# Kernel tuning notes

Hardware: AMD Instinct MI355X
Metric: run time of the kernel (lower is better)

The kernel has to match this reference:

```python
import jax, jax.numpy as jnp
import numpy as np

S = 64.0   # arcface scale
M = 0.5    # arcface additive angular margin
EPS = 1e-07
B, D, C = 1024, 512, 100000


def setup_inputs() -> dict:
    key = jax.random.key(0)
    k1, k2, k3 = jax.random.split(key, 3)
    features = jax.random.normal(k1, (B, D), dtype=jnp.float32)
    # Linear(512, 100000, bias=False) weight, ~1/sqrt(512) init scale.
    W = jax.random.normal(k2, (C, D), dtype=jnp.float32) * 0.04
    y_true = jax.random.randint(k3, (B,), 0, C, dtype=jnp.int64)
    return {"features": features, "W": W, "y_true": y_true}


def reference(features, W, y_true):
    # L2-normalize features along dim=1 (torch F.normalize, eps=1e-12).
    norm = jnp.maximum(jnp.linalg.norm(features, axis=1, keepdims=True), 1e-12)
    xn = features / norm
    # NOTE: the original module's weight-normalization loop is a no-op
    # (rebinds a local), so W is used unnormalized — faithful to the source.
    wf = xn @ W.T                                   # [B, C] cosine-like logits
    tgt = wf[jnp.arange(B), y_true]                  # true-class logit per row
    # arcface: s * cos(acos(clamp(t)) + m)
    numerator = S * jnp.cos(jnp.arccos(jnp.clip(tgt, -1.0 + EPS, 1.0 - EPS)) + M)
    # exp-sum over all classes except the true one (mask instead of python-loop concat)
    not_true = jnp.arange(C)[None, :] != y_true[:, None]   # [B, C]
    excl_sum = jnp.sum(jnp.where(not_true, jnp.exp(S * wf), 0.0), axis=1)
    denominator = jnp.exp(numerator) + excl_sum
    L = numerator - jnp.log(denominator)
    return -jnp.mean(L)
```

## Files before the change

kernel.cpp:

```cpp
#include <hip/hip_runtime.h>
#include <math.h>

#define BATCH 1024
#define DIM   512
#define NCLS  100000
#define SCALE_S 64.0f
#define MARGIN  0.5f
#define EPS_REF 1e-7f
#define NBLK 782
#define MBLK 8
#define BKF8 128
#define WCVT_BLKS 25000
#define SEXP 92.332482616893656878f

typedef __attribute__((ext_vector_type(4))) float floatx4;

#if __has_builtin(__builtin_amdgcn_exp2f)
#define EXP2(x) __builtin_amdgcn_exp2f(x)
#else
#define EXP2(x) exp2f(x)
#endif

__device__ __forceinline__ void gload_lds16(const void* g, void* l) {
    __builtin_amdgcn_global_load_lds(
        (const __attribute__((address_space(1))) void*)g,
        (__attribute__((address_space(3))) void*)l, 16, 0, 0);
}

__global__ __launch_bounds__(256)
void k_cvtprep(const float* __restrict__ W,
               const float* __restrict__ features,
               const int* __restrict__ y,
               unsigned char* __restrict__ wf8,
               unsigned char* __restrict__ xf8,
               float* __restrict__ rowsum,
               float* __restrict__ tgt) {
    const int b = blockIdx.x;
    if (b < WCVT_BLKS) {
        const size_t i = ((size_t)b * 256 + threadIdx.x) * 8;
        const float4 lo = *(const float4*)(W + i);
        const float4 hi = *(const float4*)(W + i + 4);
        int p0 = __builtin_amdgcn_cvt_pk_fp8_f32(lo.x, lo.y, 0, false);
        p0     = __builtin_amdgcn_cvt_pk_fp8_f32(lo.z, lo.w, p0, true);
        int p1 = __builtin_amdgcn_cvt_pk_fp8_f32(hi.x, hi.y, 0, false);
        p1     = __builtin_amdgcn_cvt_pk_fp8_f32(hi.z, hi.w, p1, true);
        *(int2*)(wf8 + i) = make_int2(p0, p1);
    } else {
        const int row = b - WCVT_BLKS;
        const int t = threadIdx.x;
        const int lane = t & 63;
        const int wave = t >> 6;
        __shared__ float redS[4], redD[4];

        const float2 v  = *(const float2*)(features + (size_t)row * DIM + t * 2);
        const float2 wv = *(const float2*)(W + (size_t)y[row] * DIM + t * 2);
        float ss = v.x * v.x + v.y * v.y;
        float dd = v.x * wv.x + v.y * wv.y;
        #pragma unroll
        for (int m = 32; m >= 1; m >>= 1) { ss += __shfl_xor(ss, m); dd += __shfl_xor(dd, m); }
        if (lane == 0) { redS[wave] = ss; redD[wave] = dd; }
        __syncthreads();
        const float tot  = redS[0] + redS[1] + redS[2] + redS[3];
        const float dtot = redD[0] + redD[1] + redD[2] + redD[3];
        const float nrm = fmaxf(sqrtf(tot), 1e-12f);
        const float sc = SEXP / nrm;

        int pk = __builtin_amdgcn_cvt_pk_fp8_f32(v.x * sc, v.y * sc, 0, false);
        *(unsigned short*)(xf8 + (size_t)row * DIM + t * 2) = (unsigned short)(pk & 0xFFFF);

        if (t == 0) { rowsum[row] = 0.0f; tgt[row] = dtot / nrm; }
    }
}

__global__ __launch_bounds__(256)
void k_gemm_f8(const unsigned char* __restrict__ wf8,
               const unsigned char* __restrict__ xf8,
               float* __restrict__ rowsum) {
    __shared__ __align__(16) unsigned char As[128 * BKF8];
    __shared__ __align__(16) unsigned char Bs[128 * BKF8];

    const int tid  = threadIdx.x;
    const int wave = tid >> 6;
    const int lane = tid & 63;
    const int quad = lane >> 4;
    const int l15  = lane & 15;
    const int wm   = wave >> 1;
    const int wn   = wave & 1;

    const int bid = blockIdx.x;
    const int xcd = bid & 7;
    const int j   = bid >> 3;
    const int w   = xcd * NBLK + j;
    const int n_blk = w >> 3;
    const int m_blk = w & 7;
    const int n0 = n_blk * 128;
    const int m0 = m_blk * 128;

    const int rl = lane >> 3;
    const int cs = lane & 7;
    const unsigned char* a_src[4];
    const unsigned char* b_src[4];
    unsigned char* a_dst[4];
    unsigned char* b_dst[4];
    #pragma unroll
    for (int i = 0; i < 4; ++i) {
        const int r = wave * 32 + i * 8 + rl;
        a_src[i] = xf8 + (size_t)(m0 + r) * DIM + (cs ^ rl) * 16;
        int n = n0 + r;
        if (n > NCLS - 1) n = NCLS - 1;
        b_src[i] = wf8 + (size_t)n * DIM + (cs ^ rl) * 16;
        a_dst[i] = &As[(wave * 32 + i * 8) * BKF8];
        b_dst[i] = &Bs[(wave * 32 + i * 8) * BKF8];
    }

    int aoff[4], boff[4];
    #pragma unroll
    for (int mi = 0; mi < 4; ++mi) {
        const int r = wm * 64 + mi * 16 + l15;
        aoff[mi] = r * BKF8 + (((quad >> 1) ^ (r & 7)) * 16) + (quad & 1) * 8;
    }
    #pragma unroll
    for (int ni = 0; ni < 4; ++ni) {
        const int r = wn * 64 + ni * 16 + l15;
        boff[ni] = r * BKF8 + (((quad >> 1) ^ (r & 7)) * 16) + (quad & 1) * 8;
    }

    floatx4 acc[4][4];
    #pragma unroll
    for (int i = 0; i < 4; ++i)
        #pragma unroll
        for (int jj = 0; jj < 4; ++jj)
            acc[i][jj] = (floatx4){0.f, 0.f, 0.f, 0.f};

    for (int kt = 0; kt < DIM / BKF8; ++kt) {
        __syncthreads();
        #pragma unroll
        for (int i = 0; i < 4; ++i) {
            gload_lds16(a_src[i] + kt * BKF8, a_dst[i]);
            gload_lds16(b_src[i] + kt * BKF8, b_dst[i]);
        }
        __syncthreads();

        #pragma unroll
        for (int kc = 0; kc < 4; ++kc) {
            long a[4], b[4];
            #pragma unroll
            for (int mi = 0; mi < 4; ++mi)
                a[mi] = *(const long*)(&As[aoff[mi] ^ (kc << 5)]);
            #pragma unroll
            for (int ni = 0; ni < 4; ++ni)
                b[ni] = *(const long*)(&Bs[boff[ni] ^ (kc << 5)]);
            #pragma unroll
            for (int mi = 0; mi < 4; ++mi)
                #pragma unroll
                for (int ni = 0; ni < 4; ++ni)
                    acc[mi][ni] = __builtin_amdgcn_mfma_f32_16x16x32_fp8_fp8(
                        a[mi], b[ni], acc[mi][ni], 0, 0, 0);
        }
    }

    const bool full = (n0 + 128 <= NCLS);
    #pragma unroll
    for (int mi = 0; mi < 4; ++mi) {
        #pragma unroll
        for (int reg = 0; reg < 4; ++reg) {
            float p = 0.f;
            if (full) {
                #pragma unroll
                for (int ni = 0; ni < 4; ++ni)
                    p += EXP2(acc[mi][ni][reg]);
            } else {
                #pragma unroll
                for (int ni = 0; ni < 4; ++ni) {
                    const int n = n0 + wn * 64 + ni * 16 + l15;
                    if (n < NCLS) p += EXP2(acc[mi][ni][reg]);
                }
            }
            p += __shfl_xor(p, 1);
            p += __shfl_xor(p, 2);
            p += __shfl_xor(p, 4);
            p += __shfl_xor(p, 8);
            if (l15 == 0) {
                const int m = m0 + wm * 64 + mi * 16 + quad * 4 + reg;
                atomicAdd(&rowsum[m], p);
            }
        }
    }
}

__global__ void k_finalize(const float* __restrict__ rowsum,
                           const float* __restrict__ tgt,
                           float* __restrict__ out) {
    const int tid = threadIdx.x;
    const int lane = tid & 63;
    const int wave = tid >> 6;
    __shared__ float red[4];

    float s = 0.f;
    #pragma unroll
    for (int i = 0; i < 4; ++i) {
        const int b = tid + i * 256;
        const float traw = tgt[b];
        const float tc = fminf(fmaxf(traw, -1.0f + EPS_REF), 1.0f - EPS_REF);
        const float num = SCALE_S * cosf(acosf(tc) + MARGIN);
        const float excl = rowsum[b] - expf(SCALE_S * traw);
        const float denom = expf(num) + excl;
        s += num - logf(denom);
    }
    #pragma unroll
    for (int m = 32; m >= 1; m >>= 1) s += __shfl_xor(s, m);
    if (lane == 0) red[wave] = s;
    __syncthreads();
    if (tid == 0)
        out[0] = -(red[0] + red[1] + red[2] + red[3]) / (float)BATCH;
}

extern "C" void kernel_launch(void* const* d_in, const int* in_sizes, int n_in,
                              void* d_out, int out_size, void* d_ws, size_t ws_size,
                              hipStream_t stream) {
    const float* features = (const float*)d_in[0];
    const float* W        = (const float*)d_in[1];
    const int*   y        = (const int*)d_in[2];
    float* out = (float*)d_out;

    const size_t WF8_BYTES = (size_t)NCLS * DIM;
    const size_t XF8_BYTES = (size_t)BATCH * DIM;
    char* ws = (char*)d_ws;
    unsigned char* wf8 = (unsigned char*)ws;
    unsigned char* xf8 = (unsigned char*)(ws + WF8_BYTES);
    float* rowsum = (float*)(ws + WF8_BYTES + XF8_BYTES);
    float* tgt    = (float*)(ws + WF8_BYTES + XF8_BYTES + 4096);

    k_cvtprep<<<WCVT_BLKS + BATCH, 256, 0, stream>>>(W, features, y,
                                                     wf8, xf8, rowsum, tgt);
    k_gemm_f8<<<NBLK * MBLK, 256, 0, stream>>>(wf8, xf8, rowsum);
    k_finalize<<<1, 256, 0, stream>>>(rowsum, tgt, out);
}
```

Measured before the change: 453.3 us.

## Fuse W fp8 conversion into GEMM with LDS-resident weight slabs

Removes the separate pass that converts W to fp8 and writes it back to a workspace. Each GEMM block now loads a 64-row slab of fp32 W, converts it to fp8 in LDS once, and keeps it resident while it streams all 1024 feature rows through a double-buffered LDS tile. This avoids writing and re-reading the 51 MB fp8 copy of W, so W's fp32 bytes are read only once. In exchange, every block re-reads the whole fp8 feature matrix, the tiles are smaller (64 columns, 2x4 MFMAs per wave), and each block issues more atomics.

```diff
diff --git a/kernel.cpp b/kernel.cpp
--- a/kernel.cpp
+++ b/kernel.cpp
@@ -7,11 +7,14 @@
 #define SCALE_S 64.0f
 #define MARGIN  0.5f
 #define EPS_REF 1e-7f
-#define NBLK 782
-#define MBLK 8
-#define BKF8 128
-#define WCVT_BLKS 25000
 #define SEXP 92.332482616893656878f
+
+#define NSLAB 64
+#define NBLK  1563
+#define BK    64
+#define NKT   8
+#define MROWS 128
+#define NMT   8
 
 typedef __attribute__((ext_vector_type(4))) float floatx4;
 
@@ -28,161 +31,158 @@
 }
 
 __global__ __launch_bounds__(256)
-void k_cvtprep(const float* __restrict__ W,
-               const float* __restrict__ features,
-               const int* __restrict__ y,
-               unsigned char* __restrict__ wf8,
-               unsigned char* __restrict__ xf8,
-               float* __restrict__ rowsum,
-               float* __restrict__ tgt) {
-    const int b = blockIdx.x;
-    if (b < WCVT_BLKS) {
-        const size_t i = ((size_t)b * 256 + threadIdx.x) * 8;
-        const float4 lo = *(const float4*)(W + i);
-        const float4 hi = *(const float4*)(W + i + 4);
-        int p0 = __builtin_amdgcn_cvt_pk_fp8_f32(lo.x, lo.y, 0, false);
-        p0     = __builtin_amdgcn_cvt_pk_fp8_f32(lo.z, lo.w, p0, true);
-        int p1 = __builtin_amdgcn_cvt_pk_fp8_f32(hi.x, hi.y, 0, false);
-        p1     = __builtin_amdgcn_cvt_pk_fp8_f32(hi.z, hi.w, p1, true);
-        *(int2*)(wf8 + i) = make_int2(p0, p1);
-    } else {
-        const int row = b - WCVT_BLKS;
-        const int t = threadIdx.x;
-        const int lane = t & 63;
-        const int wave = t >> 6;
-        __shared__ float redS[4], redD[4];
-
-        const float2 v  = *(const float2*)(features + (size_t)row * DIM + t * 2);
-        const float2 wv = *(const float2*)(W + (size_t)y[row] * DIM + t * 2);
-        float ss = v.x * v.x + v.y * v.y;
-        float dd = v.x * wv.x + v.y * wv.y;
-        #pragma unroll
-        for (int m = 32; m >= 1; m >>= 1) { ss += __shfl_xor(ss, m); dd += __shfl_xor(dd, m); }
-        if (lane == 0) { redS[wave] = ss; redD[wave] = dd; }
-        __syncthreads();
-        const float tot  = redS[0] + redS[1] + redS[2] + redS[3];
-        const float dtot = redD[0] + redD[1] + redD[2] + redD[3];
-        const float nrm = fmaxf(sqrtf(tot), 1e-12f);
-        const float sc = SEXP / nrm;
-
-        int pk = __builtin_amdgcn_cvt_pk_fp8_f32(v.x * sc, v.y * sc, 0, false);
-        *(unsigned short*)(xf8 + (size_t)row * DIM + t * 2) = (unsigned short)(pk & 0xFFFF);
-
-        if (t == 0) { rowsum[row] = 0.0f; tgt[row] = dtot / nrm; }
-    }
-}
-
-__global__ __launch_bounds__(256)
-void k_gemm_f8(const unsigned char* __restrict__ wf8,
-               const unsigned char* __restrict__ xf8,
-               float* __restrict__ rowsum) {
-    __shared__ __align__(16) unsigned char As[128 * BKF8];
-    __shared__ __align__(16) unsigned char Bs[128 * BKF8];
+void k_prep(const float* __restrict__ features,
+            const float* __restrict__ W,
+            const int* __restrict__ y,
+            unsigned char* __restrict__ xf8,
+            float* __restrict__ rowsum,
+            float* __restrict__ tgt) {
+    const int row = blockIdx.x;
+    const int t = threadIdx.x;
+    const int lane = t & 63;
+    const int wave = t >> 6;
+    __shared__ float redS[4], redD[4];
+
+    const float2 v  = *(const float2*)(features + (size_t)row * DIM + t * 2);
+    const float2 wv = *(const float2*)(W + (size_t)y[row] * DIM + t * 2);
+    float ss = v.x * v.x + v.y * v.y;
+    float dd = v.x * wv.x + v.y * wv.y;
+    #pragma unroll
+    for (int m = 32; m >= 1; m >>= 1) { ss += __shfl_xor(ss, m); dd += __shfl_xor(dd, m); }
+    if (lane == 0) { redS[wave] = ss; redD[wave] = dd; }
+    __syncthreads();
+    const float tot  = redS[0] + redS[1] + redS[2] + redS[3];
+    const float dtot = redD[0] + redD[1] + redD[2] + redD[3];
+    const float nrm = fmaxf(sqrtf(tot), 1e-12f);
+    const float sc = SEXP / nrm;
+
+    int pk = __builtin_amdgcn_cvt_pk_fp8_f32(v.x * sc, v.y * sc, 0, false);
+    *(unsigned short*)(xf8 + (size_t)row * DIM + t * 2) = (unsigned short)(pk & 0xFFFF);
+
+    if (t == 0) { rowsum[row] = 0.0f; tgt[row] = dtot / nrm; }
+}
+
+__global__ __launch_bounds__(256, 3)
+void k_gemm_fused(const float* __restrict__ W,
+                  const unsigned char* __restrict__ xf8,
+                  float* __restrict__ rowsum) {
+    __shared__ __align__(16) unsigned char Ws[NSLAB * DIM];
+    __shared__ __align__(16) unsigned char As[2][MROWS * BK];
 
     const int tid  = threadIdx.x;
     const int wave = tid >> 6;
     const int lane = tid & 63;
     const int quad = lane >> 4;
     const int l15  = lane & 15;
-    const int wm   = wave >> 1;
-    const int wn   = wave & 1;
-
-    const int bid = blockIdx.x;
-    const int xcd = bid & 7;
-    const int j   = bid >> 3;
-    const int w   = xcd * NBLK + j;
-    const int n_blk = w >> 3;
-    const int m_blk = w & 7;
-    const int n0 = n_blk * 128;
-    const int m0 = m_blk * 128;
-
-    const int rl = lane >> 3;
-    const int cs = lane & 7;
-    const unsigned char* a_src[4];
-    const unsigned char* b_src[4];
-    unsigned char* a_dst[4];
-    unsigned char* b_dst[4];
-    #pragma unroll
-    for (int i = 0; i < 4; ++i) {
-        const int r = wave * 32 + i * 8 + rl;
-        a_src[i] = xf8 + (size_t)(m0 + r) * DIM + (cs ^ rl) * 16;
-        int n = n0 + r;
-        if (n > NCLS - 1) n = NCLS - 1;
-        b_src[i] = wf8 + (size_t)n * DIM + (cs ^ rl) * 16;
-        a_dst[i] = &As[(wave * 32 + i * 8) * BKF8];
-        b_dst[i] = &Bs[(wave * 32 + i * 8) * BKF8];
-    }
-
-    int aoff[4], boff[4];
-    #pragma unroll
-    for (int mi = 0; mi < 4; ++mi) {
-        const int r = wm * 64 + mi * 16 + l15;
-        aoff[mi] = r * BKF8 + (((quad >> 1) ^ (r & 7)) * 16) + (quad & 1) * 8;
+    const int n0   = blockIdx.x * NSLAB;
+
+    const int arl = lane >> 2;
+    const int acs = lane & 3;
+    const unsigned char* a_src_base =
+        xf8 + (size_t)arl * DIM + ((acs ^ (arl & 3)) << 4);
+
+    #pragma unroll
+    for (int q = 0; q < 2; ++q)
+        gload_lds16(a_src_base + (size_t)((q * 4 + wave) * 16) * DIM,
+                    &As[0][(q * 4 + wave) * 16 * BK]);
+
+    #pragma unroll
+    for (int j = 0; j < 8; ++j) {
+        const int c  = j * 256 + tid;
+        const int r  = c >> 5;
+        const int cs = c & 31;
+        int rg = n0 + r; if (rg > NCLS - 1) rg = NCLS - 1;
+        const float4* s4 = (const float4*)(W + (size_t)rg * DIM + cs * 16);
+        const float4 f0 = s4[0], f1 = s4[1], f2 = s4[2], f3 = s4[3];
+        int w0 = __builtin_amdgcn_cvt_pk_fp8_f32(f0.x, f0.y, 0, false);
+        w0     = __builtin_amdgcn_cvt_pk_fp8_f32(f0.z, f0.w, w0, true);
+        int w1 = __builtin_amdgcn_cvt_pk_fp8_f32(f1.x, f1.y, 0, false);
+        w1     = __builtin_amdgcn_cvt_pk_fp8_f32(f1.z, f1.w, w1, true);
+        int w2 = __builtin_amdgcn_cvt_pk_fp8_f32(f2.x, f2.y, 0, false);
+        w2     = __builtin_amdgcn_cvt_pk_fp8_f32(f2.z, f2.w, w2, true);
+        int w3 = __builtin_amdgcn_cvt_pk_fp8_f32(f3.x, f3.y, 0, false);
+        w3     = __builtin_amdgcn_cvt_pk_fp8_f32(f3.z, f3.w, w3, true);
+        *(int4*)(&Ws[r * DIM + ((cs ^ (r & 7)) << 4)]) = make_int4(w0, w1, w2, w3);
+    }
+
+    int aoff[2], boff[4];
+    #pragma unroll
+    for (int mi = 0; mi < 2; ++mi) {
+        const int r = wave * 32 + mi * 16 + l15;
+        aoff[mi] = r * BK + (((quad >> 1) ^ (r & 3)) << 4) + ((quad & 1) << 3);
     }
     #pragma unroll
     for (int ni = 0; ni < 4; ++ni) {
-        const int r = wn * 64 + ni * 16 + l15;
-        boff[ni] = r * BKF8 + (((quad >> 1) ^ (r & 7)) * 16) + (quad & 1) * 8;
-    }
-
-    floatx4 acc[4][4];
-    #pragma unroll
-    for (int i = 0; i < 4; ++i)
+        const int r = ni * 16 + l15;
+        boff[ni] = r * DIM + (((quad >> 1) ^ (r & 7)) << 4) + ((quad & 1) << 3);
+    }
+
+    floatx4 acc[2][4];
+    int buf = 0;
+    const bool full = (n0 + NSLAB <= NCLS);
+
+    for (int mt = 0; mt < NMT; ++mt) {
         #pragma unroll
-        for (int jj = 0; jj < 4; ++jj)
-            acc[i][jj] = (floatx4){0.f, 0.f, 0.f, 0.f};
-
-    for (int kt = 0; kt < DIM / BKF8; ++kt) {
-        __syncthreads();
-        #pragma unroll
-        for (int i = 0; i < 4; ++i) {
-            gload_lds16(a_src[i] + kt * BKF8, a_dst[i]);
-            gload_lds16(b_src[i] + kt * BKF8, b_dst[i]);
-        }
-        __syncthreads();
-
-        #pragma unroll
-        for (int kc = 0; kc < 4; ++kc) {
-            long a[4], b[4];
-            #pragma unroll
-            for (int mi = 0; mi < 4; ++mi)
-                a[mi] = *(const long*)(&As[aoff[mi] ^ (kc << 5)]);
+        for (int mi = 0; mi < 2; ++mi)
             #pragma unroll
             for (int ni = 0; ni < 4; ++ni)
-                b[ni] = *(const long*)(&Bs[boff[ni] ^ (kc << 5)]);
+                acc[mi][ni] = (floatx4){0.f, 0.f, 0.f, 0.f};
+
+        for (int kt = 0; kt < NKT; ++kt) {
+            __syncthreads();
+            const bool last = (kt == NKT - 1);
+            if (!last || mt < NMT - 1) {
+                const int nmt = last ? mt + 1 : mt;
+                const int nkt = last ? 0 : kt + 1;
+                #pragma unroll
+                for (int q = 0; q < 2; ++q)
+                    gload_lds16(a_src_base
+                                  + (size_t)(nmt * MROWS + (q * 4 + wave) * 16) * DIM
+                                  + nkt * BK,
+                                &As[buf ^ 1][(q * 4 + wave) * 16 * BK]);
+            }
             #pragma unroll
-            for (int mi = 0; mi < 4; ++mi)
+            for (int kc = 0; kc < 2; ++kc) {
+                long a[2], b[4];
+                #pragma unroll
+                for (int mi = 0; mi < 2; ++mi)
+                    a[mi] = *(const long*)(&As[buf][aoff[mi] ^ (kc << 5)]);
                 #pragma unroll
                 for (int ni = 0; ni < 4; ++ni)
-                    acc[mi][ni] = __builtin_amdgcn_mfma_f32_16x16x32_fp8_fp8(
-                        a[mi], b[ni], acc[mi][ni], 0, 0, 0);
+                    b[ni] = *(const long*)(&Ws[boff[ni] ^ (kt << 6) ^ (kc << 5)]);
+                #pragma unroll
+                for (int mi = 0; mi < 2; ++mi)
+                    #pragma unroll
+                    for (int ni = 0; ni < 4; ++ni)
+                        acc[mi][ni] = __builtin_amdgcn_mfma_f32_16x16x32_fp8_fp8(
+                            a[mi], b[ni], acc[mi][ni], 0, 0, 0);
+            }
+            buf ^= 1;
         }
-    }
-
-    const bool full = (n0 + 128 <= NCLS);
-    #pragma unroll
-    for (int mi = 0; mi < 4; ++mi) {
+
         #pragma unroll
-        for (int reg = 0; reg < 4; ++reg) {
-            float p = 0.f;
-            if (full) {
-                #pragma unroll
-                for (int ni = 0; ni < 4; ++ni)
-                    p += EXP2(acc[mi][ni][reg]);
-            } else {
-                #pragma unroll
-                for (int ni = 0; ni < 4; ++ni) {
-                    const int n = n0 + wn * 64 + ni * 16 + l15;
-                    if (n < NCLS) p += EXP2(acc[mi][ni][reg]);
+        for (int mi = 0; mi < 2; ++mi) {
+            #pragma unroll
+            for (int reg = 0; reg < 4; ++reg) {
+                float p = 0.f;
+                if (full) {
+                    p = EXP2(acc[mi][0][reg]) + EXP2(acc[mi][1][reg])
+                      + EXP2(acc[mi][2][reg]) + EXP2(acc[mi][3][reg]);
+                } else {
+                    #pragma unroll
+                    for (int ni = 0; ni < 4; ++ni) {
+                        const int n = n0 + ni * 16 + l15;
+                        if (n < NCLS) p += EXP2(acc[mi][ni][reg]);
+                    }
                 }
-            }
-            p += __shfl_xor(p, 1);
-            p += __shfl_xor(p, 2);
-            p += __shfl_xor(p, 4);
-            p += __shfl_xor(p, 8);
-            if (l15 == 0) {
-                const int m = m0 + wm * 64 + mi * 16 + quad * 4 + reg;
-                atomicAdd(&rowsum[m], p);
+                p += __shfl_xor(p, 1);
+                p += __shfl_xor(p, 2);
+                p += __shfl_xor(p, 4);
+                p += __shfl_xor(p, 8);
+                if (l15 == 0) {
+                    const int m = mt * MROWS + wave * 32 + mi * 16 + quad * 4 + reg;
+                    atomicAdd(&rowsum[m], p);
+                }
             }
         }
     }
@@ -223,16 +223,13 @@
     const int*   y        = (const int*)d_in[2];
     float* out = (float*)d_out;
 
-    const size_t WF8_BYTES = (size_t)NCLS * DIM;
     const size_t XF8_BYTES = (size_t)BATCH * DIM;
     char* ws = (char*)d_ws;
-    unsigned char* wf8 = (unsigned char*)ws;
-    unsigned char* xf8 = (unsigned char*)(ws + WF8_BYTES);
-    float* rowsum = (float*)(ws + WF8_BYTES + XF8_BYTES);
-    float* tgt    = (float*)(ws + WF8_BYTES + XF8_BYTES + 4096);
-
-    k_cvtprep<<<WCVT_BLKS + BATCH, 256, 0, stream>>>(W, features, y,
-                                                     wf8, xf8, rowsum, tgt);
-    k_gemm_f8<<<NBLK * MBLK, 256, 0, stream>>>(wf8, xf8, rowsum);
+    unsigned char* xf8 = (unsigned char*)ws;
+    float* rowsum = (float*)(ws + XF8_BYTES);
+    float* tgt    = (float*)(ws + XF8_BYTES + 4096);
+
+    k_prep<<<BATCH, 256, 0, stream>>>(features, W, y, xf8, rowsum, tgt);
+    k_gemm_fused<<<NBLK, 256, 0, stream>>>(W, xf8, rowsum);
     k_finalize<<<1, 256, 0, stream>>>(rowsum, tgt, out);
 }
```

Measured after the change: 583.3 us. +28.7%, slower.
